# Performance work log

Measured on AMD Instinct MI355X. Metric: run time of the kernel, lower is better.

## Reference

```python
import jax, jax.numpy as jnp
import numpy as np


def setup_inputs() -> dict:
    key = jax.random.key(0)
    k1, k2, k3 = jax.random.split(key, 3)
    B, S_enc, S_dec, D = 8, 4096, 4096, 128
    b = jax.random.normal(k1, (B, S_enc, D), dtype=jnp.float32)
    h = jax.random.normal(k2, (B, S_dec, D), dtype=jnp.float32)
    W_b = jax.random.normal(k3, (D, D), dtype=jnp.float32) * (1.0 / np.sqrt(D))
    return {"b": b, "h": h, "W_b": W_b}


def reference(b, h, W_b):
    # tmp1 = h @ W_b : [B, S_dec, D]
    tmp1 = jnp.einsum('btd,de->bte', h, W_b)
    # scores = tmp1 @ b^T : [B, S_dec, S_enc]
    scores = jnp.einsum('bte,bse->bts', tmp1, b)
    attn = jax.nn.softmax(scores, axis=-1)
    # weighted sum over encoder positions (the original does this via a huge
    # tile/broadcast/multiply/reduce_sum; math is a batched matmul)
    cxt = jnp.einsum('bts,bsd->btd', attn, b)
    return cxt
```

## Files before the change

### kernel.cpp

```cpp
#include <hip/hip_runtime.h>

typedef _Float16 half2v __attribute__((ext_vector_type(2)));
typedef __fp16 fp16x2 __attribute__((ext_vector_type(2)));
typedef _Float16 half4 __attribute__((ext_vector_type(4)));
typedef _Float16 half8 __attribute__((ext_vector_type(8)));
typedef float floatx4 __attribute__((ext_vector_type(4)));

#define B_   8
#define SE   4096
#define SD   4096
#define D_   128
#define NT   64
#define LDB  136
#define LOG2E 1.44269504f

__device__ __forceinline__ void cp16_async(const _Float16* g, _Float16* l) {
    __builtin_amdgcn_global_load_lds((const __attribute__((address_space(1))) unsigned int*)g,
                                     (__attribute__((address_space(3))) unsigned int*)l, 16, 0, 0);
}

__global__ __launch_bounds__(256) void wprep(const float* __restrict__ W,
                                             _Float16* __restrict__ W16,
                                             _Float16* __restrict__ Wlo) {
    int i = blockIdx.x * 256 + threadIdx.x;
    float w = W[i];
    _Float16 hi = (_Float16)w;
    W16[i] = hi;
    Wlo[i] = (_Float16)(w - (float)hi);
}

__global__ __launch_bounds__(256) void kvprep(const float* __restrict__ b,
                                              const _Float16* __restrict__ W16,
                                              const _Float16* __restrict__ Wlo,
                                              _Float16* __restrict__ kp,
                                              _Float16* __restrict__ vT) {
    __shared__ _Float16 bs[64 * LDB];
    const int bb = blockIdx.y, s0 = blockIdx.x * 64;
    const int tid = threadIdx.x, wave = tid >> 6, lane = tid & 63;
    const int l15 = lane & 15, quad = lane >> 4;

    const float* bg = b + ((size_t)bb * SE + s0) * D_;
    #pragma unroll
    for (int it = 0; it < 4; ++it) {
        int idx = tid + it * 256;
        int row = idx >> 4, seg = idx & 15;
        const float* src = bg + row * D_ + seg * 8;
        float4 a = *(const float4*)src;
        float4 c = *(const float4*)(src + 4);
        half8 hv;
        hv[0] = (_Float16)a.x; hv[1] = (_Float16)a.y; hv[2] = (_Float16)a.z; hv[3] = (_Float16)a.w;
        hv[4] = (_Float16)c.x; hv[5] = (_Float16)c.y; hv[6] = (_Float16)c.z; hv[7] = (_Float16)c.w;
        *(half8*)(bs + row * LDB + seg * 8) = hv;
    }
    __syncthreads();

    half8 af[4];
    #pragma unroll
    for (int ks = 0; ks < 4; ++ks)
        af[ks] = *(const half8*)(bs + (wave * 16 + l15) * LDB + ks * 32 + quad * 8);
    floatx4 acc[8];
    #pragma unroll
    for (int nt = 0; nt < 8; ++nt) acc[nt] = (floatx4){0.f, 0.f, 0.f, 0.f};
    #pragma unroll
    for (int ks = 0; ks < 4; ++ks) {
        #pragma unroll
        for (int nt = 0; nt < 8; ++nt) {
            half8 bh = *(const half8*)(W16 + (size_t)(nt * 16 + l15) * 128 + ks * 32 + quad * 8);
            half8 bl = *(const half8*)(Wlo + (size_t)(nt * 16 + l15) * 128 + ks * 32 + quad * 8);
            acc[nt] = __builtin_amdgcn_mfma_f32_16x16x32_f16(af[ks], bh, acc[nt], 0, 0, 0);
            acc[nt] = __builtin_amdgcn_mfma_f32_16x16x32_f16(af[ks], bl, acc[nt], 0, 0, 0);
        }
    }

    if (tid < 128) {
        const int sb = tid & 7, dg = tid >> 3;
        half8 rowv[8];
        #pragma unroll
        for (int j = 0; j < 8; ++j)
            rowv[j] = *(const half8*)(bs + (sb * 8 + j) * LDB + dg * 8);
        #pragma unroll
        for (int r = 0; r < 8; ++r) {
            int d = dg * 8 + r;
            half8 o;
            #pragma unroll
            for (int j = 0; j < 8; ++j) o[j] = rowv[j][r];
            *(half8*)(vT + ((size_t)bb * D_ + d) * SE + s0 + sb * 8) = o;
        }
    }
    __syncthreads();

    #pragma unroll
    for (int nt = 0; nt < 8; ++nt)
        #pragma unroll
        for (int r = 0; r < 4; ++r)
            bs[(wave * 16 + quad * 4 + r) * LDB + nt * 16 + l15] = (_Float16)acc[nt][r];
    __syncthreads();
    _Float16* kg = kp + ((size_t)bb * SE + s0) * D_;
    {
        const int row = tid >> 2;
        #pragma unroll
        for (int it = 0; it < 4; ++it) {
            int ch = (tid & 3) + it * 4;
            half8 v = *(const half8*)(bs + row * LDB + ch * 8);
            *(half8*)(kg + row * D_ + ch * 8) = v;
        }
    }
}

__global__ __launch_bounds__(256, 2) void flash(const float* __restrict__ h,
                                                const _Float16* __restrict__ k,
                                                const _Float16* __restrict__ vT,
                                                float* __restrict__ out) {
    __shared__ _Float16 KV[2][16384];

    const int bb   = blockIdx.y;
    const int q0   = blockIdx.x * 64;
    const int tid  = threadIdx.x;
    const int wave = tid >> 6;
    const int lane = tid & 63;
    const int l15  = lane & 15;
    const int quad = lane >> 4;

    const _Float16* kbase = k + (size_t)bb * SE * D_;
    const _Float16* vbase = vT + (size_t)bb * D_ * SE;

    int koff[4], voff[4];
    #pragma unroll
    for (int j = 0; j < 4; ++j) {
        int i = (wave * 4 + j) * 64 + lane;
        int kr = i >> 4, kpp = i & 15;
        koff[j] = kr * D_ + (kpp ^ (kr & 15)) * 8;
        int vr = i >> 3, vpp = i & 7;
        voff[j] = vr * SE + (vpp ^ (vr & 7)) * 8;
    }

    const _Float16* kA0[4]; const _Float16* kA1[4];
    const _Float16* vB0[4]; const _Float16* vB1[4];
    #pragma unroll
    for (int ks = 0; ks < 4; ++ks) {
        int o = l15 * 128 + (((ks * 4 + quad) ^ l15) * 8);
        kA0[ks] = &KV[0][o]; kA1[ks] = &KV[1][o];
    }
    #pragma unroll
    for (int st = 0; st < 4; ++st) {
        int o = 8192 + l15 * 64 + (((st * 2 + (quad >> 1)) ^ (l15 & 7)) * 8) + (quad & 1) * 4;
        vB0[st] = &KV[0][o]; vB1[st] = &KV[1][o];
    }

    {
        _Float16* buf0 = &KV[0][0];
        #pragma unroll
        for (int j = 0; j < 4; ++j) {
            cp16_async(kbase + koff[j], buf0 + (wave * 4 + j) * 512);
            cp16_async(vbase + voff[j], buf0 + 8192 + (wave * 4 + j) * 512);
        }
    }

    const float* hrow = h + ((size_t)bb * SD + q0 + wave * 16 + l15) * D_;
    half8 qf[4];
    #pragma unroll
    for (int ks = 0; ks < 4; ++ks) {
        float4 a = *(const float4*)(hrow + ks * 32 + quad * 8);
        float4 c = *(const float4*)(hrow + ks * 32 + quad * 8 + 4);
        half8 f;
        f[0] = (_Float16)(a.x * LOG2E); f[1] = (_Float16)(a.y * LOG2E);
        f[2] = (_Float16)(a.z * LOG2E); f[3] = (_Float16)(a.w * LOG2E);
        f[4] = (_Float16)(c.x * LOG2E); f[5] = (_Float16)(c.y * LOG2E);
        f[6] = (_Float16)(c.z * LOG2E); f[7] = (_Float16)(c.w * LOG2E);
        qf[ks] = f;
    }

    floatx4 acc_o[8];
    #pragma unroll
    for (int i = 0; i < 8; ++i) acc_o[i] = (floatx4){0.f, 0.f, 0.f, 0.f};
    float m_q = -1e30f;
    float l_part = 0.f;
    const half2v one2 = { (_Float16)1.f, (_Float16)1.f };

    for (int t = 0; t < SE / NT; ++t) {
        __syncthreads();
        if (t + 1 < SE / NT) {
            const _Float16* kt = kbase + (size_t)(t + 1) * (NT * D_);
            const _Float16* vt = vbase + (size_t)(t + 1) * NT;
            _Float16* bufn = &KV[(t + 1) & 1][0];
            #pragma unroll
            for (int j = 0; j < 4; ++j) {
                cp16_async(kt + koff[j], bufn + (wave * 4 + j) * 512);
                cp16_async(vt + voff[j], bufn + 8192 + (wave * 4 + j) * 512);
            }
        }
        const bool odd = (t & 1) != 0;
        const _Float16* kA[4]; const _Float16* vB[4];
        #pragma unroll
        for (int i = 0; i < 4; ++i) { kA[i] = odd ? kA1[i] : kA0[i]; vB[i] = odd ? vB1[i] : vB0[i]; }

        floatx4 accs[4];
        #pragma unroll
        for (int st = 0; st < 4; ++st) accs[st] = (floatx4){0.f, 0.f, 0.f, 0.f};
        #pragma unroll
        for (int ks = 0; ks < 4; ++ks) {
            #pragma unroll
            for (int st = 0; st < 4; ++st) {
                half8 af = *(const half8*)(kA[ks] + st * 2048);
                accs[st] = __builtin_amdgcn_mfma_f32_16x16x32_f16(af, qf[ks], accs[st], 0, 0, 0);
            }
        }

        float mx[8];
        #pragma unroll
        for (int i = 0; i < 8; ++i) mx[i] = fmaxf(accs[i >> 1][(i & 1) * 2], accs[i >> 1][(i & 1) * 2 + 1]);
        float m4a = fmaxf(fmaxf(mx[0], mx[1]), fmaxf(mx[2], mx[3]));
        float m4b = fmaxf(fmaxf(mx[4], mx[5]), fmaxf(mx[6], mx[7]));
        float mv16 = fmaxf(m4a, m4b);
        bool cond = mv16 > m_q + 11.5f;
        if (__ballot(cond) != 0ull) {
            float mv = mv16;
            mv = fmaxf(mv, __shfl_xor(mv, 16, 64));
            mv = fmaxf(mv, __shfl_xor(mv, 32, 64));
            float mnew = fmaxf(m_q, mv);
            float alpha = exp2f(m_q - mnew);
            l_part *= alpha;
            float ab[4];
            #pragma unroll
            for (int r = 0; r < 4; ++r) ab[r] = __shfl(alpha, quad * 4 + r, 64);
            #pragma unroll
            for (int dt = 0; dt < 8; ++dt)
                #pragma unroll
                for (int r = 0; r < 4; ++r) acc_o[dt][r] *= ab[r];
            m_q = mnew;
        }

        half4 pf[4];
        #pragma unroll
        for (int st = 0; st < 4; ++st) {
            float p0 = exp2f(accs[st][0] - m_q);
            float p1 = exp2f(accs[st][1] - m_q);
            float p2 = exp2f(accs[st][2] - m_q);
            float p3 = exp2f(accs[st][3] - m_q);
            half2v lo = __builtin_bit_cast(half2v, __builtin_amdgcn_cvt_pkrtz(p0, p1));
            half2v hi = __builtin_bit_cast(half2v, __builtin_amdgcn_cvt_pkrtz(p2, p3));
#if __has_builtin(__builtin_amdgcn_fdot2)
            l_part = __builtin_amdgcn_fdot2(lo, one2, l_part, false);
            l_part = __builtin_amdgcn_fdot2(hi, one2, l_part, false);
#else
            l_part += p0 + p1 + p2 + p3;
#endif
            half4 pv; pv[0] = lo[0]; pv[1] = lo[1]; pv[2] = hi[0]; pv[3] = hi[1];
            pf[st] = pv;
        }

        #pragma unroll
        for (int st = 0; st < 4; ++st) {
            #pragma unroll
            for (int dt = 0; dt < 8; ++dt) {
                half4 vf = *(const half4*)(vB[st] + dt * 1024);
                acc_o[dt] = __builtin_amdgcn_mfma_f32_16x16x16f16(pf[st], vf, acc_o[dt], 0, 0, 0);
            }
        }
    }

    l_part += __shfl_xor(l_part, 16, 64);
    l_part += __shfl_xor(l_part, 32, 64);
    float linv = 1.f / l_part;
    float lb[4];
    #pragma unroll
    for (int r = 0; r < 4; ++r) lb[r] = __shfl(linv, quad * 4 + r, 64);
    float* orow = out + ((size_t)bb * SD + q0 + wave * 16) * D_;
    #pragma unroll
    for (int dt = 0; dt < 8; ++dt)
        #pragma unroll
        for (int r = 0; r < 4; ++r)
            orow[(size_t)(quad * 4 + r) * D_ + dt * 16 + l15] = acc_o[dt][r] * lb[r];
}

extern "C" void kernel_launch(void* const* d_in, const int* in_sizes, int n_in,
                              void* d_out, int out_size, void* d_ws, size_t ws_size,
                              hipStream_t stream) {
    const float* b = (const float*)d_in[0];
    const float* h = (const float*)d_in[1];
    const float* W = (const float*)d_in[2];
    float* out = (float*)d_out;

    _Float16* W16 = (_Float16*)d_ws;
    _Float16* Wlo = W16 + 128 * 128;
    _Float16* kp  = Wlo + 128 * 128;
    _Float16* vT  = kp + (size_t)B_ * SE * D_;

    wprep<<<64, 256, 0, stream>>>(W, W16, Wlo);
    kvprep<<<dim3(SE / 64, B_), 256, 0, stream>>>(b, W16, Wlo, kp, vT);
    flash<<<dim3(SD / 64, B_), 256, 0, stream>>>(h, kp, vT, out);
}
```

Before: 213.2 us.

## Split each KV tile across wave pairs with two query tiles per wave

The flash kernel now gives each pair of waves the same 32 query rows and splits each 64-key tile between the two waves. Each wave covers 32 keys for two 16-row query tiles, so every K and V fragment read from LDS feeds two MFMAs, which roughly halves LDS read traffic per MFMA. A cross-wave merge through LDS at the end combines the two partial softmax states. The change costs more accumulator registers (two sets of output tiles), which could lower occupancy. The V-transpose in kvprep is also reworked so all 256 threads write half4 chunks instead of 128 threads writing half8.

```diff
diff --git a/kernel.cpp b/kernel.cpp
--- a/kernel.cpp
+++ b/kernel.cpp
@@ -1,7 +1,6 @@
 #include <hip/hip_runtime.h>
 
 typedef _Float16 half2v __attribute__((ext_vector_type(2)));
-typedef __fp16 fp16x2 __attribute__((ext_vector_type(2)));
 typedef _Float16 half4 __attribute__((ext_vector_type(4)));
 typedef _Float16 half8 __attribute__((ext_vector_type(8)));
 typedef float floatx4 __attribute__((ext_vector_type(4)));
@@ -72,19 +71,19 @@
         }
     }
 
-    if (tid < 128) {
-        const int sb = tid & 7, dg = tid >> 3;
-        half8 rowv[8];
-        #pragma unroll
-        for (int j = 0; j < 8; ++j)
-            rowv[j] = *(const half8*)(bs + (sb * 8 + j) * LDB + dg * 8);
+    {
+        const int sq = tid & 15, dg = tid >> 4;
+        half8 rowv[4];
+        #pragma unroll
+        for (int j = 0; j < 4; ++j)
+            rowv[j] = *(const half8*)(bs + (sq * 4 + j) * LDB + dg * 8);
         #pragma unroll
         for (int r = 0; r < 8; ++r) {
             int d = dg * 8 + r;
-            half8 o;
-            #pragma unroll
-            for (int j = 0; j < 8; ++j) o[j] = rowv[j][r];
-            *(half8*)(vT + ((size_t)bb * D_ + d) * SE + s0 + sb * 8) = o;
+            half4 o;
+            #pragma unroll
+            for (int j = 0; j < 4; ++j) o[j] = rowv[j][r];
+            *(half4*)(vT + ((size_t)bb * D_ + d) * SE + s0 + sq * 4) = o;
         }
     }
     __syncthreads();
@@ -117,6 +116,8 @@
     const int q0   = blockIdx.x * 64;
     const int tid  = threadIdx.x;
     const int wave = tid >> 6;
+    const int wq   = wave >> 1;
+    const int ws   = wave & 1;
     const int lane = tid & 63;
     const int l15  = lane & 15;
     const int quad = lane >> 4;
@@ -135,16 +136,16 @@
     }
 
     const _Float16* kA0[4]; const _Float16* kA1[4];
-    const _Float16* vB0[4]; const _Float16* vB1[4];
+    const _Float16* vB0[2]; const _Float16* vB1[2];
     #pragma unroll
     for (int ks = 0; ks < 4; ++ks) {
-        int o = l15 * 128 + (((ks * 4 + quad) ^ l15) * 8);
+        int o = l15 * 128 + (((ks * 4 + quad) ^ l15) * 8) + ws * 4096;
         kA0[ks] = &KV[0][o]; kA1[ks] = &KV[1][o];
     }
     #pragma unroll
-    for (int st = 0; st < 4; ++st) {
-        int o = 8192 + l15 * 64 + (((st * 2 + (quad >> 1)) ^ (l15 & 7)) * 8) + (quad & 1) * 4;
-        vB0[st] = &KV[0][o]; vB1[st] = &KV[1][o];
+    for (int stl = 0; stl < 2; ++stl) {
+        int o = 8192 + l15 * 64 + (((ws * 4 + stl * 2 + (quad >> 1)) ^ (l15 & 7)) * 8) + (quad & 1) * 4;
+        vB0[stl] = &KV[0][o]; vB1[stl] = &KV[1][o];
     }
 
     {
@@ -156,25 +157,30 @@
         }
     }
 
-    const float* hrow = h + ((size_t)bb * SD + q0 + wave * 16 + l15) * D_;
-    half8 qf[4];
-    #pragma unroll
-    for (int ks = 0; ks < 4; ++ks) {
-        float4 a = *(const float4*)(hrow + ks * 32 + quad * 8);
-        float4 c = *(const float4*)(hrow + ks * 32 + quad * 8 + 4);
-        half8 f;
-        f[0] = (_Float16)(a.x * LOG2E); f[1] = (_Float16)(a.y * LOG2E);
-        f[2] = (_Float16)(a.z * LOG2E); f[3] = (_Float16)(a.w * LOG2E);
-        f[4] = (_Float16)(c.x * LOG2E); f[5] = (_Float16)(c.y * LOG2E);
-        f[6] = (_Float16)(c.z * LOG2E); f[7] = (_Float16)(c.w * LOG2E);
-        qf[ks] = f;
-    }
-
-    floatx4 acc_o[8];
-    #pragma unroll
-    for (int i = 0; i < 8; ++i) acc_o[i] = (floatx4){0.f, 0.f, 0.f, 0.f};
-    float m_q = -1e30f;
-    float l_part = 0.f;
+    half8 qf[2][4];
+    #pragma unroll
+    for (int qt = 0; qt < 2; ++qt) {
+        const float* hrow = h + ((size_t)bb * SD + q0 + wq * 32 + qt * 16 + l15) * D_;
+        #pragma unroll
+        for (int ks = 0; ks < 4; ++ks) {
+            float4 a = *(const float4*)(hrow + ks * 32 + quad * 8);
+            float4 c = *(const float4*)(hrow + ks * 32 + quad * 8 + 4);
+            half8 f;
+            f[0] = (_Float16)(a.x * LOG2E); f[1] = (_Float16)(a.y * LOG2E);
+            f[2] = (_Float16)(a.z * LOG2E); f[3] = (_Float16)(a.w * LOG2E);
+            f[4] = (_Float16)(c.x * LOG2E); f[5] = (_Float16)(c.y * LOG2E);
+            f[6] = (_Float16)(c.z * LOG2E); f[7] = (_Float16)(c.w * LOG2E);
+            qf[qt][ks] = f;
+        }
+    }
+
+    floatx4 acc_o[2][8];
+    #pragma unroll
+    for (int qt = 0; qt < 2; ++qt)
+        #pragma unroll
+        for (int dt = 0; dt < 8; ++dt) acc_o[qt][dt] = (floatx4){0.f, 0.f, 0.f, 0.f};
+    float m_q[2] = {-1e30f, -1e30f};
+    float l_part[2] = {0.f, 0.f};
     const half2v one2 = { (_Float16)1.f, (_Float16)1.f };
 
     for (int t = 0; t < SE / NT; ++t) {
@@ -190,87 +196,141 @@
             }
         }
         const bool odd = (t & 1) != 0;
-        const _Float16* kA[4]; const _Float16* vB[4];
-        #pragma unroll
-        for (int i = 0; i < 4; ++i) { kA[i] = odd ? kA1[i] : kA0[i]; vB[i] = odd ? vB1[i] : vB0[i]; }
-
-        floatx4 accs[4];
-        #pragma unroll
-        for (int st = 0; st < 4; ++st) accs[st] = (floatx4){0.f, 0.f, 0.f, 0.f};
+        const _Float16* kA[4]; const _Float16* vB[2];
+        #pragma unroll
+        for (int i = 0; i < 4; ++i) kA[i] = odd ? kA1[i] : kA0[i];
+        #pragma unroll
+        for (int i = 0; i < 2; ++i) vB[i] = odd ? vB1[i] : vB0[i];
+
+        floatx4 accs[2][2];
+        #pragma unroll
+        for (int stl = 0; stl < 2; ++stl)
+            #pragma unroll
+            for (int qt = 0; qt < 2; ++qt) accs[stl][qt] = (floatx4){0.f, 0.f, 0.f, 0.f};
         #pragma unroll
         for (int ks = 0; ks < 4; ++ks) {
-            #pragma unroll
-            for (int st = 0; st < 4; ++st) {
-                half8 af = *(const half8*)(kA[ks] + st * 2048);
-                accs[st] = __builtin_amdgcn_mfma_f32_16x16x32_f16(af, qf[ks], accs[st], 0, 0, 0);
-            }
-        }
-
-        float mx[8];
-        #pragma unroll
-        for (int i = 0; i < 8; ++i) mx[i] = fmaxf(accs[i >> 1][(i & 1) * 2], accs[i >> 1][(i & 1) * 2 + 1]);
-        float m4a = fmaxf(fmaxf(mx[0], mx[1]), fmaxf(mx[2], mx[3]));
-        float m4b = fmaxf(fmaxf(mx[4], mx[5]), fmaxf(mx[6], mx[7]));
-        float mv16 = fmaxf(m4a, m4b);
-        bool cond = mv16 > m_q + 11.5f;
+            half8 af0 = *(const half8*)(kA[ks]);
+            half8 af1 = *(const half8*)(kA[ks] + 2048);
+            accs[0][0] = __builtin_amdgcn_mfma_f32_16x16x32_f16(af0, qf[0][ks], accs[0][0], 0, 0, 0);
+            accs[0][1] = __builtin_amdgcn_mfma_f32_16x16x32_f16(af0, qf[1][ks], accs[0][1], 0, 0, 0);
+            accs[1][0] = __builtin_amdgcn_mfma_f32_16x16x32_f16(af1, qf[0][ks], accs[1][0], 0, 0, 0);
+            accs[1][1] = __builtin_amdgcn_mfma_f32_16x16x32_f16(af1, qf[1][ks], accs[1][1], 0, 0, 0);
+        }
+
+        float mv[2];
+        #pragma unroll
+        for (int qt = 0; qt < 2; ++qt) {
+            float a = fmaxf(fmaxf(accs[0][qt][0], accs[0][qt][1]), fmaxf(accs[0][qt][2], accs[0][qt][3]));
+            float b2 = fmaxf(fmaxf(accs[1][qt][0], accs[1][qt][1]), fmaxf(accs[1][qt][2], accs[1][qt][3]));
+            mv[qt] = fmaxf(a, b2);
+        }
+        bool cond = (mv[0] > m_q[0] + 11.5f) || (mv[1] > m_q[1] + 11.5f);
         if (__ballot(cond) != 0ull) {
-            float mv = mv16;
-            mv = fmaxf(mv, __shfl_xor(mv, 16, 64));
-            mv = fmaxf(mv, __shfl_xor(mv, 32, 64));
-            float mnew = fmaxf(m_q, mv);
-            float alpha = exp2f(m_q - mnew);
-            l_part *= alpha;
-            float ab[4];
-            #pragma unroll
-            for (int r = 0; r < 4; ++r) ab[r] = __shfl(alpha, quad * 4 + r, 64);
+            #pragma unroll
+            for (int qt = 0; qt < 2; ++qt) {
+                float m = mv[qt];
+                m = fmaxf(m, __shfl_xor(m, 16, 64));
+                m = fmaxf(m, __shfl_xor(m, 32, 64));
+                float mnew = fmaxf(m_q[qt], m);
+                float alpha = exp2f(m_q[qt] - mnew);
+                l_part[qt] *= alpha;
+                float ab[4];
+                #pragma unroll
+                for (int r = 0; r < 4; ++r) ab[r] = __shfl(alpha, quad * 4 + r, 64);
+                #pragma unroll
+                for (int dt = 0; dt < 8; ++dt)
+                    #pragma unroll
+                    for (int r = 0; r < 4; ++r) acc_o[qt][dt][r] *= ab[r];
+                m_q[qt] = mnew;
+            }
+        }
+
+        half4 pf[2][2];
+        #pragma unroll
+        for (int qt = 0; qt < 2; ++qt)
+            #pragma unroll
+            for (int stl = 0; stl < 2; ++stl) {
+                float p0 = exp2f(accs[stl][qt][0] - m_q[qt]);
+                float p1 = exp2f(accs[stl][qt][1] - m_q[qt]);
+                float p2 = exp2f(accs[stl][qt][2] - m_q[qt]);
+                float p3 = exp2f(accs[stl][qt][3] - m_q[qt]);
+                half2v lo = __builtin_bit_cast(half2v, __builtin_amdgcn_cvt_pkrtz(p0, p1));
+                half2v hi = __builtin_bit_cast(half2v, __builtin_amdgcn_cvt_pkrtz(p2, p3));
+#if __has_builtin(__builtin_amdgcn_fdot2)
+                l_part[qt] = __builtin_amdgcn_fdot2(lo, one2, l_part[qt], false);
+                l_part[qt] = __builtin_amdgcn_fdot2(hi, one2, l_part[qt], false);
+#else
+                l_part[qt] += p0 + p1 + p2 + p3;
+#endif
+                half4 pv; pv[0] = lo[0]; pv[1] = lo[1]; pv[2] = hi[0]; pv[3] = hi[1];
+                pf[qt][stl] = pv;
+            }
+
+        #pragma unroll
+        for (int stl = 0; stl < 2; ++stl) {
+            #pragma unroll
+            for (int dt = 0; dt < 8; ++dt) {
+                half4 vf = *(const half4*)(vB[stl] + dt * 1024);
+                acc_o[0][dt] = __builtin_amdgcn_mfma_f32_16x16x16f16(pf[0][stl], vf, acc_o[0][dt], 0, 0, 0);
+                acc_o[1][dt] = __builtin_amdgcn_mfma_f32_16x16x16f16(pf[1][stl], vf, acc_o[1][dt], 0, 0, 0);
+            }
+        }
+    }
+
+    float l_own[2];
+    #pragma unroll
+    for (int qt = 0; qt < 2; ++qt) {
+        float l = l_part[qt];
+        l += __shfl_xor(l, 16, 64);
+        l += __shfl_xor(l, 32, 64);
+        l_own[qt] = l;
+    }
+
+    __syncthreads();
+    float* Ob = (float*)&KV[0][0];
+    float* ml = (float*)&KV[0][0] + 8192;
+
+    if (ws == 1) {
+        #pragma unroll
+        for (int qt = 0; qt < 2; ++qt) {
             #pragma unroll
             for (int dt = 0; dt < 8; ++dt)
+                *(floatx4*)(Ob + (((wq * 2 + qt) * 8 + dt) * 64 + lane) * 4) = acc_o[qt][dt];
+            if (quad == 0)
+                *(float2*)(ml + (wq * 32 + qt * 16 + l15) * 2) = make_float2(m_q[qt], l_own[qt]);
+        }
+    }
+    __syncthreads();
+    if (ws == 0) {
+        #pragma unroll
+        for (int qt = 0; qt < 2; ++qt) {
+            float m0r[4], l0r[4], m1r[4], l1r[4];
+            #pragma unroll
+            for (int r = 0; r < 4; ++r) {
+                m0r[r] = __shfl(m_q[qt], quad * 4 + r, 64);
+                l0r[r] = __shfl(l_own[qt], quad * 4 + r, 64);
+                float2 p = *(float2*)(ml + (wq * 32 + qt * 16 + quad * 4 + r) * 2);
+                m1r[r] = p.x; l1r[r] = p.y;
+            }
+            float a0[4], a1[4], inv[4];
+            #pragma unroll
+            for (int r = 0; r < 4; ++r) {
+                float mm = fmaxf(m0r[r], m1r[r]);
+                a0[r] = exp2f(m0r[r] - mm);
+                a1[r] = exp2f(m1r[r] - mm);
+                inv[r] = 1.f / (l0r[r] * a0[r] + l1r[r] * a1[r]);
+            }
+            float* orow = out + ((size_t)bb * SD + q0 + wq * 32 + qt * 16 + quad * 4) * D_;
+            #pragma unroll
+            for (int dt = 0; dt < 8; ++dt) {
+                floatx4 o1 = *(floatx4*)(Ob + (((wq * 2 + qt) * 8 + dt) * 64 + lane) * 4);
                 #pragma unroll
-                for (int r = 0; r < 4; ++r) acc_o[dt][r] *= ab[r];
-            m_q = mnew;
-        }
-
-        half4 pf[4];
-        #pragma unroll
-        for (int st = 0; st < 4; ++st) {
-            float p0 = exp2f(accs[st][0] - m_q);
-            float p1 = exp2f(accs[st][1] - m_q);
-            float p2 = exp2f(accs[st][2] - m_q);
-            float p3 = exp2f(accs[st][3] - m_q);
-            half2v lo = __builtin_bit_cast(half2v, __builtin_amdgcn_cvt_pkrtz(p0, p1));
-            half2v hi = __builtin_bit_cast(half2v, __builtin_amdgcn_cvt_pkrtz(p2, p3));
-#if __has_builtin(__builtin_amdgcn_fdot2)
-            l_part = __builtin_amdgcn_fdot2(lo, one2, l_part, false);
-            l_part = __builtin_amdgcn_fdot2(hi, one2, l_part, false);
-#else
-            l_part += p0 + p1 + p2 + p3;
-#endif
-            half4 pv; pv[0] = lo[0]; pv[1] = lo[1]; pv[2] = hi[0]; pv[3] = hi[1];
-            pf[st] = pv;
-        }
-
-        #pragma unroll
-        for (int st = 0; st < 4; ++st) {
-            #pragma unroll
-            for (int dt = 0; dt < 8; ++dt) {
-                half4 vf = *(const half4*)(vB[st] + dt * 1024);
-                acc_o[dt] = __builtin_amdgcn_mfma_f32_16x16x16f16(pf[st], vf, acc_o[dt], 0, 0, 0);
-            }
-        }
-    }
-
-    l_part += __shfl_xor(l_part, 16, 64);
-    l_part += __shfl_xor(l_part, 32, 64);
-    float linv = 1.f / l_part;
-    float lb[4];
-    #pragma unroll
-    for (int r = 0; r < 4; ++r) lb[r] = __shfl(linv, quad * 4 + r, 64);
-    float* orow = out + ((size_t)bb * SD + q0 + wave * 16) * D_;
-    #pragma unroll
-    for (int dt = 0; dt < 8; ++dt)
-        #pragma unroll
-        for (int r = 0; r < 4; ++r)
-            orow[(size_t)(quad * 4 + r) * D_ + dt * 16 + l15] = acc_o[dt][r] * lb[r];
+                for (int r = 0; r < 4; ++r)
+                    orow[(size_t)r * D_ + dt * 16 + l15] =
+                        (acc_o[qt][dt][r] * a0[r] + o1[r] * a1[r]) * inv[r];
+            }
+        }
+    }
 }
 
 extern "C" void kernel_launch(void* const* d_in, const int* in_sizes, int n_in,
```

New measurement: 215.9 us. No clear change (+1.3%).
